# Optimization experiments

Measured on AMD Instinct MI355X. Metric: run time of the kernel, lower is better.

Reference implementation:

```python
import jax, jax.numpy as jnp
import numpy as np
from jax import lax

D_MODEL = 1024
D_STATE = 16
D_CONV = 4
D_INNER = 2 * D_MODEL
BATCH = 2
SEQ = 1024


def setup_inputs() -> dict:
    key = jax.random.key(0)
    ks = jax.random.split(key, 8)
    std = 0.02
    return {
        "x": jax.random.normal(ks[0], (BATCH, SEQ, D_MODEL), jnp.float32),
        "in_proj_w": jax.random.normal(ks[1], (2 * D_INNER, D_MODEL), jnp.float32) * std,
        "conv_w": jax.random.normal(ks[2], (D_INNER, 1, D_CONV), jnp.float32) * 0.1,
        "x_proj_w": jax.random.normal(ks[3], (D_STATE + 1, D_INNER), jnp.float32) * std,
        "dt_w": jax.random.normal(ks[4], (D_INNER, 1), jnp.float32) * std,
        "dt_b": jnp.zeros((D_INNER,), jnp.float32),
        "A_param": jax.random.normal(ks[5], (D_INNER, D_STATE), jnp.float32) * std,
        "D_param": jnp.ones((D_INNER,), jnp.float32),
        "out_w": jax.random.normal(ks[6], (D_MODEL, D_INNER), jnp.float32) * std,
        "out_b": jnp.zeros((D_MODEL,), jnp.float32),
    }


def _silu(v):
    return v * jax.nn.sigmoid(v)


def _mamba_forward(x, in_proj_w, conv_w, x_proj_w, dt_w, dt_b, A_param, D_param, out_w, out_b):
    B, L, _ = x.shape
    # in_proj: [B,L,2*d_inner]
    xz = jnp.einsum('bld,ed->ble', x, in_proj_w)
    u, z = jnp.split(xz, 2, axis=-1)  # each [B,L,d_inner]
    # depthwise causal conv1d along time
    uc = u.transpose(0, 2, 1)  # [B,d_inner,L]
    uc = lax.conv_general_dilated(
        uc, conv_w, window_strides=(1,), padding=[(D_CONV - 1, D_CONV - 1)],
        dimension_numbers=('NCH', 'OIH', 'NCH'), feature_group_count=D_INNER,
    )[:, :, :L]
    u = _silu(uc.transpose(0, 2, 1))  # [B,L,d_inner]
    # x_proj -> (dt scalar, B coeffs)
    x_dbl = jnp.einsum('bld,ed->ble', u, x_proj_w)  # [B,L,d_state+1]
    dt_in = x_dbl[..., :1]                          # [B,L,1]
    Bmat = x_dbl[..., 1:]                           # [B,L,d_state]
    delta = jax.nn.softplus(dt_in * dt_w[:, 0] + dt_b)  # [B,L,d_inner]
    A = -jnp.exp(A_param)                            # [d_inner,d_state]

    # selective scan (time-major lax.scan)
    def step(h, inp):
        d_t, b_t = inp  # [B,d_inner], [B,d_state]
        h = jnp.exp(A * d_t[..., None]) * h + d_t[..., None] * b_t[:, None, :]
        y = jnp.einsum('bdn,bn->bd', h, b_t)
        return h, y

    h0 = jnp.zeros((B, D_INNER, D_STATE), x.dtype)
    _, ys = lax.scan(step, h0, (delta.transpose(1, 0, 2), Bmat.transpose(1, 0, 2)))
    y = ys.transpose(1, 0, 2) + u * D_param  # [B,L,d_inner]
    y = y * _silu(z)
    return jnp.einsum('bld,ed->ble', y, out_w) + out_b


def reference(x, in_proj_w, conv_w, x_proj_w, dt_w, dt_b, A_param, D_param, out_w, out_b):
    return _mamba_forward(x, in_proj_w, conv_w, x_proj_w, dt_w, dt_b, A_param, D_param, out_w, out_b)
```

## Files before the change

kernel.cpp:

```cpp
#include <hip/hip_runtime.h>
#include <stdint.h>
#include <stddef.h>

#define D_MODEL 1024
#define D_STATE 16
#define D_INNER 2048
#define BATCH   2
#define SEQ     1024
#define MROWS   (BATCH*SEQ)

#define NCH 32
#define TCH (SEQ/NCH)
#define NREC (BATCH*D_INNER*D_STATE)

#define XKS 8
#define XKC (D_INNER/XKS)

typedef __bf16 bf16x8 __attribute__((ext_vector_type(8)));
typedef float  f32x4  __attribute__((ext_vector_type(4)));
typedef unsigned short u16x8 __attribute__((ext_vector_type(8)));

__device__ __forceinline__ unsigned short f2bf(float f) {
    unsigned int u = __float_as_uint(f);
    u += 0x7fffu + ((u >> 16) & 1u);
    return (unsigned short)(u >> 16);
}
__device__ __forceinline__ float bf2f(unsigned short v) {
    return __uint_as_float((unsigned int)v << 16);
}

__device__ __forceinline__ void gl_lds16(const unsigned short* g, unsigned short* l) {
    __builtin_amdgcn_global_load_lds(
        (const __attribute__((address_space(1))) unsigned int*)g,
        (__attribute__((address_space(3))) unsigned int*)l, 16, 0, 0);
}

__global__ void cvt_all_kernel(const float* __restrict__ x,
                               const float* __restrict__ w1,
                               const float* __restrict__ w2,
                               const float* __restrict__ xw,
                               unsigned short* __restrict__ xb,
                               unsigned short* __restrict__ wbi,
                               unsigned short* __restrict__ wbo,
                               unsigned short* __restrict__ wbp) {
    int blk = blockIdx.x, tid = threadIdx.x;
    if (blk < 8192) {
        const float* src; unsigned short* dst; int i;
        if (blk < 2048)      { src = x;  dst = xb;  i = blk * 1024 + tid * 4; }
        else if (blk < 6144) { src = w1; dst = wbi; i = (blk - 2048) * 1024 + tid * 4; }
        else                 { src = w2; dst = wbo; i = (blk - 6144) * 1024 + tid * 4; }
        float4 v = *(const float4*)(src + i);
        ushort4 o;
        o.x = f2bf(v.x); o.y = f2bf(v.y); o.z = f2bf(v.z); o.w = f2bf(v.w);
        *(ushort4*)(dst + i) = o;
    } else {
        int id = (blk - 8192) * 256 + tid;
        wbp[id] = (id < 17 * D_INNER) ? f2bf(xw[id]) : (unsigned short)0;
    }
}

template<int NT, bool SPLITK2, bool OUT_BF16>
__global__ void gemm_bf16_kernel(const unsigned short* __restrict__ A,
                                 const unsigned short* __restrict__ Bw,
                                 void* __restrict__ Cv,
                                 int M, int N, int K) {
    constexpr int NTW = NT / 32;
    constexpr int BCH = NT / 8;
    __shared__ __align__(16) unsigned short Al[2][2 * 128 * 32];
    __shared__ __align__(16) unsigned short Bl[2][2 * NT * 32];

    const int tid  = threadIdx.x;
    const int lane = tid & 63;
    const int wid  = tid >> 6;
    const int wm   = wid >> 1;
    const int wn   = wid & 1;
    const int ln   = lane & 15;
    const int q    = lane >> 4;
    const int mblk = blockIdx.y * 128;
    const int nblk = blockIdx.x * NT;
    const int srow = lane >> 2;
    const int spart = lane & 3;

    const int kbeg = SPLITK2 ? blockIdx.z * (K / 2) : 0;
    const int kend = SPLITK2 ? kbeg + K / 2 : K;

    f32x4 acc[4][NTW] = {};

    auto stage = [&](int buf, int k0) {
        #pragma unroll
        for (int h = 0; h < 4; ++h) {
            int j = wid * 4 + h;
            int kh = j & 1, rb = j >> 1;
            int row = rb * 16 + srow;
            gl_lds16(A + (size_t)(mblk + row) * K + k0 + kh * 32 + spart * 8,
                     Al[buf] + kh * 4096 + rb * 512);
        }
        #pragma unroll
        for (int h = 0; h < BCH / 4; ++h) {
            int j = wid * (BCH / 4) + h;
            int kh = j & 1, rb = j >> 1;
            int row = rb * 16 + srow;
            gl_lds16(Bw + (size_t)(nblk + row) * K + k0 + kh * 32 + spart * 8,
                     Bl[buf] + kh * (NT * 32) + rb * 512);
        }
    };

    stage(0, kbeg);
    __syncthreads();
    int cur = 0;

    for (int k0 = kbeg; k0 < kend; k0 += 64) {
        if (k0 + 64 < kend) stage(cur ^ 1, k0 + 64);

        #pragma unroll
        for (int kh = 0; kh < 2; ++kh) {
            bf16x8 af[4], bfr[NTW];
            #pragma unroll
            for (int mt = 0; mt < 4; ++mt)
                af[mt] = *(const bf16x8*)(Al[cur] + kh * 4096 + (wm * 64 + mt * 16 + ln) * 32 + q * 8);
            #pragma unroll
            for (int nt = 0; nt < NTW; ++nt)
                bfr[nt] = *(const bf16x8*)(Bl[cur] + kh * (NT * 32) + (wn * (NT/2) + nt * 16 + ln) * 32 + q * 8);
            #pragma unroll
            for (int mt = 0; mt < 4; ++mt)
                #pragma unroll
                for (int nt = 0; nt < NTW; ++nt)
                    acc[mt][nt] = __builtin_amdgcn_mfma_f32_16x16x32_bf16(
                        af[mt], bfr[nt], acc[mt][nt], 0, 0, 0);
        }
        __syncthreads();
        cur ^= 1;
    }

    size_t cofs = SPLITK2 ? (size_t)blockIdx.z * M * N : 0;
    #pragma unroll
    for (int mt = 0; mt < 4; ++mt) {
        #pragma unroll
        for (int nt = 0; nt < NTW; ++nt) {
            int col = nblk + wn * (NT/2) + nt * 16 + ln;
            #pragma unroll
            for (int r = 0; r < 4; ++r) {
                int row = mblk + wm * 64 + mt * 16 + q * 4 + r;
                if (OUT_BF16)
                    ((unsigned short*)Cv)[cofs + (size_t)row * N + col] = f2bf(acc[mt][nt][r]);
                else
                    ((float*)Cv)[cofs + (size_t)row * N + col] = acc[mt][nt][r];
            }
        }
    }
}

__global__ void splitk_reduce_kernel(const float* __restrict__ part,
                                     const float* __restrict__ bias,
                                     float* __restrict__ out) {
    int i = (blockIdx.x * 256 + threadIdx.x) * 4;
    int n = i & (D_MODEL - 1);
    float4 a = *(const float4*)(part + i);
    float4 b = *(const float4*)(part + (size_t)MROWS * D_MODEL + i);
    float4 bv = *(const float4*)(bias + n);
    float4 o;
    o.x = a.x + b.x + bv.x; o.y = a.y + b.y + bv.y;
    o.z = a.z + b.z + bv.z; o.w = a.w + b.w + bv.w;
    *(float4*)(out + i) = o;
}

__global__ void conv_silu_kernel(const unsigned short* __restrict__ xzb,
                                 const float* __restrict__ conv_w,
                                 unsigned short* __restrict__ ub) {
    int idx = blockIdx.x * 256 + threadIdx.x;
    int d8 = idx & 255;
    int m = idx >> 8;
    int l = m & (SEQ - 1);
    int d = d8 * 8;
    const float4* wv = (const float4*)(conv_w + (size_t)d * 4);
    float4 w[8];
    #pragma unroll
    for (int e = 0; e < 8; ++e) w[e] = wv[e];
    float s[8] = {0.f, 0.f, 0.f, 0.f, 0.f, 0.f, 0.f, 0.f};
    #pragma unroll
    for (int j = 0; j < 4; ++j) {
        if (l - j >= 0) {
            u16x8 r = *(const u16x8*)(xzb + (size_t)(m - j) * 4096 + d);
            #pragma unroll
            for (int e = 0; e < 8; ++e) {
                float wt = (j == 0) ? w[e].w : (j == 1) ? w[e].z
                         : (j == 2) ? w[e].y : w[e].x;
                s[e] += wt * bf2f(r[e]);
            }
        }
    }
    u16x8 o;
    #pragma unroll
    for (int e = 0; e < 8; ++e) {
        float sig = 1.f / (1.f + __expf(-s[e]));
        o[e] = f2bf(s[e] * sig);
    }
    *(u16x8*)(ub + (size_t)m * D_INNER + d) = o;
}

__global__ void xproj_mfma_kernel(const unsigned short* __restrict__ ub,
                                  const unsigned short* __restrict__ wbp,
                                  float* __restrict__ part) {
    __shared__ __align__(16) unsigned short Al[2][64 * 64];
    __shared__ __align__(16) unsigned short Bl[2][32 * 64];

    const int tid  = threadIdx.x;
    const int lane = tid & 63;
    const int wid  = tid >> 6;
    const int ln   = lane & 15;
    const int q    = lane >> 4;
    const int m0   = blockIdx.y * 64;
    const int ks   = blockIdx.x;
    const int srow = lane >> 3;
    const int spart = lane & 7;

    f32x4 acc[2] = {};

    auto stage = [&](int buf, int it) {
        int k0 = ks * XKC + it * 64;
        #pragma unroll
        for (int h = 0; h < 2; ++h) {
            int j = wid * 2 + h;
            int row = j * 8 + srow;
            gl_lds16(ub + (size_t)(m0 + row) * D_INNER + k0 + spart * 8, Al[buf] + j * 512);
        }
        {
            int row = wid * 8 + srow;
            gl_lds16(wbp + (size_t)row * D_INNER + k0 + spart * 8, Bl[buf] + wid * 512);
        }
    };

    stage(0, 0);
    __syncthreads();
    int cur = 0;

    for (int it = 0; it < 4; ++it) {
        if (it < 3) stage(cur ^ 1, it + 1);

        bf16x8 af[2], bfr[2][2];
        #pragma unroll
        for (int kh = 0; kh < 2; ++kh) {
            af[kh] = *(const bf16x8*)(Al[cur] + (wid * 16 + ln) * 64 + kh * 32 + q * 8);
            bfr[0][kh] = *(const bf16x8*)(Bl[cur] + (0 * 16 + ln) * 64 + kh * 32 + q * 8);
            bfr[1][kh] = *(const bf16x8*)(Bl[cur] + (1 * 16 + ln) * 64 + kh * 32 + q * 8);
        }
        #pragma unroll
        for (int kh = 0; kh < 2; ++kh) {
            acc[0] = __builtin_amdgcn_mfma_f32_16x16x32_bf16(af[kh], bfr[0][kh], acc[0], 0, 0, 0);
            acc[1] = __builtin_amdgcn_mfma_f32_16x16x32_bf16(af[kh], bfr[1][kh], acc[1], 0, 0, 0);
        }
        __syncthreads();
        cur ^= 1;
    }

    #pragma unroll
    for (int nf = 0; nf < 2; ++nf) {
        #pragma unroll
        for (int r = 0; r < 4; ++r) {
            int m = m0 + wid * 16 + q * 4 + r;
            part[((size_t)ks * MROWS + m) * 32 + nf * 16 + ln] = acc[nf][r];
        }
    }
}

__global__ void xproj_reduce_kernel(const float* __restrict__ part,
                                    float* __restrict__ dti,
                                    float* __restrict__ Bm) {
    int id = blockIdx.x * 256 + threadIdx.x;
    int m = id >> 5, n = id & 31;
    float s = 0.f;
    #pragma unroll
    for (int ks = 0; ks < XKS; ++ks) s += part[(size_t)ks * MROWS * 32 + id];
    if (n == 0) dti[m] = s;
    else if (n < 17) Bm[(size_t)m * D_STATE + (n - 1)] = s;
}

__device__ __forceinline__ float softplus_f(float xv) {
    return fmaxf(xv, 0.f) + __logf(1.f + __expf(-fabsf(xv)));
}

__global__ void scanA_kernel(const float* __restrict__ dt_in,
                             const float* __restrict__ Bm,
                             const float* __restrict__ dt_w,
                             const float* __restrict__ dt_b,
                             const float* __restrict__ A_param,
                             float* __restrict__ Pg,
                             float* __restrict__ Sg) {
    __shared__ float sdt[TCH];
    __shared__ float sB[TCH * D_STATE];
    const int tid = threadIdx.x;
    const int b = blockIdx.z, c = blockIdx.y;
    const int d = blockIdx.x * 256 + tid;

    if (tid < TCH) sdt[tid] = dt_in[b * SEQ + c * TCH + tid];
    if (tid < TCH * D_STATE / 4)
        ((float4*)sB)[tid] = ((const float4*)(Bm + ((size_t)(b * SEQ + c * TCH)) * D_STATE))[tid];
    __syncthreads();

    const float dtw = dt_w[d], dtb = dt_b[d];
    float aA[D_STATE], h[D_STATE];
    #pragma unroll
    for (int n4 = 0; n4 < 4; ++n4) {
        float4 ap = ((const float4*)(A_param + (size_t)d * D_STATE))[n4];
        aA[n4*4+0] = -__expf(ap.x); aA[n4*4+1] = -__expf(ap.y);
        aA[n4*4+2] = -__expf(ap.z); aA[n4*4+3] = -__expf(ap.w);
    }
    #pragma unroll
    for (int n = 0; n < D_STATE; ++n) h[n] = 0.f;
    float tsum = 0.f;

    for (int t = 0; t < TCH; ++t) {
        float sp = softplus_f(sdt[t] * dtw + dtb);
        tsum += sp;
        #pragma unroll
        for (int n = 0; n < D_STATE; ++n) {
            float a = __expf(aA[n] * sp);
            h[n] = a * h[n] + sp * sB[t * D_STATE + n];
        }
    }

    size_t base = (size_t)c * NREC + ((size_t)(b * D_INNER + d)) * D_STATE;
    #pragma unroll
    for (int n4 = 0; n4 < 4; ++n4) {
        float4 pv, sv;
        pv.x = __expf(aA[n4*4+0] * tsum); pv.y = __expf(aA[n4*4+1] * tsum);
        pv.z = __expf(aA[n4*4+2] * tsum); pv.w = __expf(aA[n4*4+3] * tsum);
        sv.x = h[n4*4+0]; sv.y = h[n4*4+1]; sv.z = h[n4*4+2]; sv.w = h[n4*4+3];
        *(float4*)(Pg + base + n4 * 4) = pv;
        *(float4*)(Sg + base + n4 * 4) = sv;
    }
}

__global__ void scanB_kernel(const float* __restrict__ Pg,
                             const float* __restrict__ Sg,
                             float* __restrict__ Hin) {
    int idx = blockIdx.x * 256 + threadIdx.x;
    float h = 0.f;
    #pragma unroll
    for (int c = 0; c < NCH; ++c) {
        size_t o = (size_t)c * NREC + idx;
        Hin[o] = h;
        h = Pg[o] * h + Sg[o];
    }
}

__global__ void scanC_kernel(const float* __restrict__ dt_in,
                             const float* __restrict__ Bm,
                             const float* __restrict__ dt_w,
                             const float* __restrict__ dt_b,
                             const float* __restrict__ A_param,
                             const float* __restrict__ Hin,
                             const unsigned short* __restrict__ ub,
                             const unsigned short* __restrict__ xzb,
                             const float* __restrict__ Dp,
                             unsigned short* __restrict__ ypb) {
    __shared__ float sdt[TCH];
    __shared__ float sB[TCH * D_STATE];
    const int tid = threadIdx.x;
    const int b = blockIdx.z, c = blockIdx.y;
    const int d = blockIdx.x * 256 + tid;

    if (tid < TCH) sdt[tid] = dt_in[b * SEQ + c * TCH + tid];
    if (tid < TCH * D_STATE / 4)
        ((float4*)sB)[tid] = ((const float4*)(Bm + ((size_t)(b * SEQ + c * TCH)) * D_STATE))[tid];
    __syncthreads();

    const float dtw = dt_w[d], dtb = dt_b[d];
    const float Dv = Dp[d];
    float aA[D_STATE], h[D_STATE];
    #pragma unroll
    for (int n4 = 0; n4 < 4; ++n4) {
        float4 ap = ((const float4*)(A_param + (size_t)d * D_STATE))[n4];
        aA[n4*4+0] = -__expf(ap.x); aA[n4*4+1] = -__expf(ap.y);
        aA[n4*4+2] = -__expf(ap.z); aA[n4*4+3] = -__expf(ap.w);
    }
    size_t hbase = (size_t)c * NREC + ((size_t)(b * D_INNER + d)) * D_STATE;
    #pragma unroll
    for (int n4 = 0; n4 < 4; ++n4) {
        float4 hv = *(const float4*)(Hin + hbase + n4 * 4);
        h[n4*4+0] = hv.x; h[n4*4+1] = hv.y; h[n4*4+2] = hv.z; h[n4*4+3] = hv.w;
    }

    const size_t mrow0 = (size_t)b * SEQ + c * TCH;
    for (int t = 0; t < TCH; ++t) {
        float sp = softplus_f(sdt[t] * dtw + dtb);
        float y0 = 0.f, y1 = 0.f, y2 = 0.f, y3 = 0.f;
        #pragma unroll
        for (int n4 = 0; n4 < 4; ++n4) {
            #pragma unroll
            for (int j = 0; j < 4; ++j) {
                int n = n4 * 4 + j;
                float Bv = sB[t * D_STATE + n];
                float a = __expf(aA[n] * sp);
                h[n] = a * h[n] + sp * Bv;
                float p = h[n] * Bv;
                if (n4 == 0) y0 += p; else if (n4 == 1) y1 += p;
                else if (n4 == 2) y2 += p; else y3 += p;
            }
        }
        float y = (y0 + y1) + (y2 + y3);
        size_t m = mrow0 + t;
        float z  = bf2f(xzb[m * 4096 + D_INNER + d]);
        float sz = z / (1.f + __expf(-z));
        float uv = bf2f(ub[m * D_INNER + d]);
        ypb[m * D_INNER + d] = f2bf((y + uv * Dv) * sz);
    }
}

extern "C" void kernel_launch(void* const* d_in, const int* in_sizes, int n_in,
                              void* d_out, int out_size, void* d_ws, size_t ws_size,
                              hipStream_t stream) {
    const float* x         = (const float*)d_in[0];
    const float* in_proj_w = (const float*)d_in[1];
    const float* conv_w    = (const float*)d_in[2];
    const float* x_proj_w  = (const float*)d_in[3];
    const float* dt_w      = (const float*)d_in[4];
    const float* dt_b      = (const float*)d_in[5];
    const float* A_param   = (const float*)d_in[6];
    const float* D_param   = (const float*)d_in[7];
    const float* out_w     = (const float*)d_in[8];
    const float* out_b     = (const float*)d_in[9];
    float* out = (float*)d_out;

    char* ws = (char*)d_ws;
    unsigned short* xb  = (unsigned short*)(ws);
    unsigned short* wbi = (unsigned short*)(ws + (4u  << 20));
    unsigned short* wbo = (unsigned short*)(ws + (12u << 20));
    unsigned short* xzb = (unsigned short*)(ws + (16u << 20));
    unsigned short* ub  = (unsigned short*)(ws + (32u << 20));
    float*          dti = (float*)(ws + (40u << 20));
    float*          Bm  = (float*)(ws + (40u << 20) + (64u  << 10));
    unsigned short* wbp = (unsigned short*)(ws + (40u << 20) + (192u << 10));
    float*          xpt = (float*)(ws + (40u << 20) + (512u << 10));
    float*          Pg  = (float*)(ws + (44u << 20));
    float*          Sg  = (float*)(ws + (52u << 20));
    float*          Hin = (float*)(ws + (60u << 20));
    unsigned short* ypb = (unsigned short*)(ws + (68u << 20));
    float*          g2p = (float*)(ws + (76u << 20));

    cvt_all_kernel<<<dim3(8448), 256, 0, stream>>>(
        x, in_proj_w, out_w, x_proj_w, xb, wbi, wbo, wbp);

    gemm_bf16_kernel<128, false, true><<<dim3(4096 / 128, MROWS / 128), 256, 0, stream>>>(
        xb, wbi, xzb, MROWS, 2 * D_INNER, D_MODEL);

    conv_silu_kernel<<<dim3(MROWS), 256, 0, stream>>>(xzb, conv_w, ub);

    xproj_mfma_kernel<<<dim3(XKS, MROWS / 64), 256, 0, stream>>>(ub, wbp, xpt);
    xproj_reduce_kernel<<<dim3(MROWS * 32 / 256), 256, 0, stream>>>(xpt, dti, Bm);

    scanA_kernel<<<dim3(D_INNER / 256, NCH, BATCH), 256, 0, stream>>>(
        dti, Bm, dt_w, dt_b, A_param, Pg, Sg);
    scanB_kernel<<<dim3(NREC / 256), 256, 0, stream>>>(Pg, Sg, Hin);
    scanC_kernel<<<dim3(D_INNER / 256, NCH, BATCH), 256, 0, stream>>>(
        dti, Bm, dt_w, dt_b, A_param, Hin, ub, xzb, D_param, ypb);

    gemm_bf16_kernel<64, true, false><<<dim3(1024 / 64, MROWS / 128, 2), 256, 0, stream>>>(
        ypb, wbo, g2p, MROWS, D_MODEL, D_INNER);

    splitk_reduce_kernel<<<dim3(MROWS * D_MODEL / 1024), 256, 0, stream>>>(g2p, out_b, out);
}
```

Baseline: 220.2 us.

## Fuse conv+SiLU with x_proj reduction and halve scan chunk count

Merges the depthwise conv/SiLU kernel with the x_proj projection, so each block computes one row's activations and immediately reduces them against the 17 projection rows with wave shuffles and a small LDS reduction. This removes the split-K MFMA x_proj kernel, its partial buffer and the separate reduce kernel, saving two launches and a round trip of ub through global memory. It also drops the scan chunk count from 32 to 16, which doubles the serial work per chunk but halves the chunk-state traffic and the scanB work. The fused projection now runs 17 shuffle reductions per thread instead of using MFMA.

```diff
diff --git a/kernel.cpp b/kernel.cpp
--- a/kernel.cpp
+++ b/kernel.cpp
@@ -9,12 +9,9 @@
 #define SEQ     1024
 #define MROWS   (BATCH*SEQ)
 
-#define NCH 32
+#define NCH 16
 #define TCH (SEQ/NCH)
 #define NREC (BATCH*D_INNER*D_STATE)
-
-#define XKS 8
-#define XKC (D_INNER/XKS)
 
 typedef __bf16 bf16x8 __attribute__((ext_vector_type(8)));
 typedef float  f32x4  __attribute__((ext_vector_type(4)));
@@ -164,14 +161,20 @@
     *(float4*)(out + i) = o;
 }
 
-__global__ void conv_silu_kernel(const unsigned short* __restrict__ xzb,
-                                 const float* __restrict__ conv_w,
-                                 unsigned short* __restrict__ ub) {
-    int idx = blockIdx.x * 256 + threadIdx.x;
-    int d8 = idx & 255;
-    int m = idx >> 8;
-    int l = m & (SEQ - 1);
-    int d = d8 * 8;
+__global__ void conv_xproj_kernel(const unsigned short* __restrict__ xzb,
+                                  const float* __restrict__ conv_w,
+                                  const unsigned short* __restrict__ wbp,
+                                  unsigned short* __restrict__ ub,
+                                  float* __restrict__ dti,
+                                  float* __restrict__ Bm) {
+    __shared__ float red[4][17];
+    const int tid = threadIdx.x;
+    const int m = blockIdx.x;
+    const int l = m & (SEQ - 1);
+    const int d = tid * 8;
+    const int lane = tid & 63;
+    const int wid  = tid >> 6;
+
     const float4* wv = (const float4*)(conv_w + (size_t)d * 4);
     float4 w[8];
     #pragma unroll
@@ -189,90 +192,33 @@
             }
         }
     }
+    float u[8];
     u16x8 o;
     #pragma unroll
     for (int e = 0; e < 8; ++e) {
         float sig = 1.f / (1.f + __expf(-s[e]));
-        o[e] = f2bf(s[e] * sig);
+        u[e] = s[e] * sig;
+        o[e] = f2bf(u[e]);
     }
     *(u16x8*)(ub + (size_t)m * D_INNER + d) = o;
-}
-
-__global__ void xproj_mfma_kernel(const unsigned short* __restrict__ ub,
-                                  const unsigned short* __restrict__ wbp,
-                                  float* __restrict__ part) {
-    __shared__ __align__(16) unsigned short Al[2][64 * 64];
-    __shared__ __align__(16) unsigned short Bl[2][32 * 64];
-
-    const int tid  = threadIdx.x;
-    const int lane = tid & 63;
-    const int wid  = tid >> 6;
-    const int ln   = lane & 15;
-    const int q    = lane >> 4;
-    const int m0   = blockIdx.y * 64;
-    const int ks   = blockIdx.x;
-    const int srow = lane >> 3;
-    const int spart = lane & 7;
-
-    f32x4 acc[2] = {};
-
-    auto stage = [&](int buf, int it) {
-        int k0 = ks * XKC + it * 64;
-        #pragma unroll
-        for (int h = 0; h < 2; ++h) {
-            int j = wid * 2 + h;
-            int row = j * 8 + srow;
-            gl_lds16(ub + (size_t)(m0 + row) * D_INNER + k0 + spart * 8, Al[buf] + j * 512);
-        }
-        {
-            int row = wid * 8 + srow;
-            gl_lds16(wbp + (size_t)row * D_INNER + k0 + spart * 8, Bl[buf] + wid * 512);
-        }
-    };
-
-    stage(0, 0);
+
+    #pragma unroll
+    for (int n = 0; n < 17; ++n) {
+        u16x8 wn = *(const u16x8*)(wbp + (size_t)n * D_INNER + d);
+        float p = 0.f;
+        #pragma unroll
+        for (int e = 0; e < 8; ++e) p += u[e] * bf2f(wn[e]);
+        #pragma unroll
+        for (int off = 32; off > 0; off >>= 1)
+            p += __shfl_xor(p, off, 64);
+        if (lane == 0) red[wid][n] = p;
+    }
     __syncthreads();
-    int cur = 0;
-
-    for (int it = 0; it < 4; ++it) {
-        if (it < 3) stage(cur ^ 1, it + 1);
-
-        bf16x8 af[2], bfr[2][2];
-        #pragma unroll
-        for (int kh = 0; kh < 2; ++kh) {
-            af[kh] = *(const bf16x8*)(Al[cur] + (wid * 16 + ln) * 64 + kh * 32 + q * 8);
-            bfr[0][kh] = *(const bf16x8*)(Bl[cur] + (0 * 16 + ln) * 64 + kh * 32 + q * 8);
-            bfr[1][kh] = *(const bf16x8*)(Bl[cur] + (1 * 16 + ln) * 64 + kh * 32 + q * 8);
-        }
-        #pragma unroll
-        for (int kh = 0; kh < 2; ++kh) {
-            acc[0] = __builtin_amdgcn_mfma_f32_16x16x32_bf16(af[kh], bfr[0][kh], acc[0], 0, 0, 0);
-            acc[1] = __builtin_amdgcn_mfma_f32_16x16x32_bf16(af[kh], bfr[1][kh], acc[1], 0, 0, 0);
-        }
-        __syncthreads();
-        cur ^= 1;
-    }
-
-    #pragma unroll
-    for (int nf = 0; nf < 2; ++nf) {
-        #pragma unroll
-        for (int r = 0; r < 4; ++r) {
-            int m = m0 + wid * 16 + q * 4 + r;
-            part[((size_t)ks * MROWS + m) * 32 + nf * 16 + ln] = acc[nf][r];
-        }
-    }
-}
-
-__global__ void xproj_reduce_kernel(const float* __restrict__ part,
-                                    float* __restrict__ dti,
-                                    float* __restrict__ Bm) {
-    int id = blockIdx.x * 256 + threadIdx.x;
-    int m = id >> 5, n = id & 31;
-    float s = 0.f;
-    #pragma unroll
-    for (int ks = 0; ks < XKS; ++ks) s += part[(size_t)ks * MROWS * 32 + id];
-    if (n == 0) dti[m] = s;
-    else if (n < 17) Bm[(size_t)m * D_STATE + (n - 1)] = s;
+    if (tid < 17) {
+        float ssum = red[0][tid] + red[1][tid] + red[2][tid] + red[3][tid];
+        if (tid == 0) dti[m] = ssum;
+        else Bm[(size_t)m * D_STATE + (tid - 1)] = ssum;
+    }
 }
 
 __device__ __forceinline__ float softplus_f(float xv) {
@@ -293,8 +239,7 @@
     const int d = blockIdx.x * 256 + tid;
 
     if (tid < TCH) sdt[tid] = dt_in[b * SEQ + c * TCH + tid];
-    if (tid < TCH * D_STATE / 4)
-        ((float4*)sB)[tid] = ((const float4*)(Bm + ((size_t)(b * SEQ + c * TCH)) * D_STATE))[tid];
+    ((float4*)sB)[tid] = ((const float4*)(Bm + ((size_t)(b * SEQ + c * TCH)) * D_STATE))[tid];
     __syncthreads();
 
     const float dtw = dt_w[d], dtb = dt_b[d];
@@ -361,8 +306,7 @@
     const int d = blockIdx.x * 256 + tid;
 
     if (tid < TCH) sdt[tid] = dt_in[b * SEQ + c * TCH + tid];
-    if (tid < TCH * D_STATE / 4)
-        ((float4*)sB)[tid] = ((const float4*)(Bm + ((size_t)(b * SEQ + c * TCH)) * D_STATE))[tid];
+    ((float4*)sB)[tid] = ((const float4*)(Bm + ((size_t)(b * SEQ + c * TCH)) * D_STATE))[tid];
     __syncthreads();
 
     const float dtw = dt_w[d], dtb = dt_b[d];
@@ -375,11 +319,13 @@
         aA[n4*4+2] = -__expf(ap.z); aA[n4*4+3] = -__expf(ap.w);
     }
     size_t hbase = (size_t)c * NREC + ((size_t)(b * D_INNER + d)) * D_STATE;
+    float h4[D_STATE];
     #pragma unroll
     for (int n4 = 0; n4 < 4; ++n4) {
         float4 hv = *(const float4*)(Hin + hbase + n4 * 4);
         h[n4*4+0] = hv.x; h[n4*4+1] = hv.y; h[n4*4+2] = hv.z; h[n4*4+3] = hv.w;
     }
+    (void)h4;
 
     const size_t mrow0 = (size_t)b * SEQ + c * TCH;
     for (int t = 0; t < TCH; ++t) {
@@ -431,7 +377,6 @@
     float*          dti = (float*)(ws + (40u << 20));
     float*          Bm  = (float*)(ws + (40u << 20) + (64u  << 10));
     unsigned short* wbp = (unsigned short*)(ws + (40u << 20) + (192u << 10));
-    float*          xpt = (float*)(ws + (40u << 20) + (512u << 10));
     float*          Pg  = (float*)(ws + (44u << 20));
     float*          Sg  = (float*)(ws + (52u << 20));
     float*          Hin = (float*)(ws + (60u << 20));
@@ -444,10 +389,7 @@
     gemm_bf16_kernel<128, false, true><<<dim3(4096 / 128, MROWS / 128), 256, 0, stream>>>(
         xb, wbi, xzb, MROWS, 2 * D_INNER, D_MODEL);
 
-    conv_silu_kernel<<<dim3(MROWS), 256, 0, stream>>>(xzb, conv_w, ub);
-
-    xproj_mfma_kernel<<<dim3(XKS, MROWS / 64), 256, 0, stream>>>(ub, wbp, xpt);
-    xproj_reduce_kernel<<<dim3(MROWS * 32 / 256), 256, 0, stream>>>(xpt, dti, Bm);
+    conv_xproj_kernel<<<dim3(MROWS), 256, 0, stream>>>(xzb, conv_w, wbp, ub, dti, Bm);
 
     scanA_kernel<<<dim3(D_INNER / 256, NCH, BATCH), 256, 0, stream>>>(
         dti, Bm, dt_w, dt_b, A_param, Pg, Sg);
```

Result: slower. 234.3 us (+6.4%).
